# Performance work log

Measured on AMD Instinct MI355X. Metric: run time of the kernel, lower is better.

## Reference

```python
import jax, jax.numpy as jnp
from jax import lax
import numpy as np

IMG_CH = 3
C = 48            # total channels
HIDDEN = 256
FIRE_RATE = 0.5
DX_NOISE = 0.0
NEG_SLOPE = 0.01  # torch LeakyReLU default


def _dwconv(x_nchw, w):
    # depthwise 3x3 conv with reflect padding, w: [C,1,3,3]
    xp = jnp.pad(x_nchw, ((0, 0), (0, 0), (1, 1), (1, 1)), mode='reflect')
    return lax.conv_general_dilated(
        xp, w, window_strides=(1, 1), padding='VALID',
        feature_group_count=C,
        dimension_numbers=('NCHW', 'OIHW', 'NCHW'))


def setup_inputs() -> dict:
    key = jax.random.key(0)
    ks = jax.random.split(key, 6)
    x = jax.random.normal(ks[0], (8, 256, 256, C), dtype=jnp.float32)
    filt0 = jax.random.normal(ks[1], (C, 1, 3, 3), dtype=jnp.float32) * 0.1
    filt1 = jax.random.normal(ks[2], (C, 1, 3, 3), dtype=jnp.float32) * 0.1
    fan_in = 3 * C
    w1 = jax.random.normal(ks[3], (HIDDEN, 3 * C), dtype=jnp.float32) / np.sqrt(fan_in).astype(np.float32)
    b1 = jax.random.normal(ks[4], (HIDDEN,), dtype=jnp.float32) * 0.01
    # original zero-inits w2; randomized small so outputs/grads are nontrivial
    w2 = jax.random.normal(ks[5], (C, HIDDEN), dtype=jnp.float32) * 0.02
    return {"x": x, "filt0": filt0, "filt1": filt1, "w1": w1, "b1": b1, "w2": w2, "steps": 4}


def reference(x, filt0, filt1, w1, b1, w2, steps):
    ch_mask = (jnp.arange(C) >= IMG_CH).astype(x.dtype)  # immutable image channels
    rng = jax.random.key(42)
    for i in range(steps):
        xc = jnp.transpose(x, (0, 3, 1, 2))                       # [B,C,H,W]
        p = jnp.concatenate([xc, _dwconv(xc, filt0), _dwconv(xc, filt1)], axis=1)
        p = jnp.transpose(p, (0, 2, 3, 1))                        # [B,H,W,3C]
        h = jax.nn.leaky_relu(jnp.einsum('bhwf,of->bhwo', p, w1) + b1, NEG_SLOPE)
        d = jnp.einsum('bhwo,co->bhwc', h, w2)                    # [B,H,W,C]
        k1, k2 = jax.random.split(jax.random.fold_in(rng, i))
        fire = (jax.random.uniform(k1, d.shape[:3] + (1,)) > FIRE_RATE).astype(d.dtype)
        d = d * fire + DX_NOISE * jax.random.normal(k2, d.shape[:3] + (1,), dtype=d.dtype)
        d = d * ch_mask
        x = x + d
    return x
```

## Files before the change

### kernel.cpp

```cpp
#include <hip/hip_runtime.h>
#include <stdint.h>
#include <stddef.h>


#define B_   8
#define H_   256
#define W_   256
#define C_   48
#define F_   144
#define HID_ 256
#define PW_  64
#define NTOT (B_*H_*W_*C_)
#define XSTR 56

typedef __attribute__((ext_vector_type(8))) short short8;
typedef __attribute__((ext_vector_type(4))) float f32x4;

struct U2 { unsigned x, y; };

__host__ __device__ __forceinline__ unsigned rotl32(unsigned v, int r) {
  return (v << r) | (v >> (32 - r));
}

__host__ __device__ __forceinline__ U2 threefry2x32(unsigned k0, unsigned k1,
                                                    unsigned x0, unsigned x1) {
  const unsigned k2 = k0 ^ k1 ^ 0x1BD11BDAu;
  x0 += k0; x1 += k1;
#define TF_R(r) { x0 += x1; x1 = rotl32(x1, r); x1 ^= x0; }
  TF_R(13) TF_R(15) TF_R(26) TF_R(6)
  x0 += k1; x1 += k2 + 1u;
  TF_R(17) TF_R(29) TF_R(16) TF_R(24)
  x0 += k2; x1 += k0 + 2u;
  TF_R(13) TF_R(15) TF_R(26) TF_R(6)
  x0 += k0; x1 += k1 + 3u;
  TF_R(17) TF_R(29) TF_R(16) TF_R(24)
  x0 += k1; x1 += k2 + 4u;
  TF_R(13) TF_R(15) TF_R(26) TF_R(6)
  x0 += k2; x1 += k0 + 5u;
#undef TF_R
  U2 r; r.x = x0; r.y = x1; return r;
}

__device__ __forceinline__ unsigned short f2bf(float f) {
  unsigned u = __float_as_uint(f);
  unsigned r = u + 0x7FFFu + ((u >> 16) & 1u);
  return (unsigned short)(r >> 16);
}
__device__ __forceinline__ unsigned packbf2(float lo, float hi) {
  return (unsigned)f2bf(lo) | ((unsigned)f2bf(hi) << 16);
}
__device__ __forceinline__ float bf2f(unsigned short u) {
  return __uint_as_float(((unsigned)u) << 16);
}

#define W1B_N 114688
#define W2B_N 12288
__global__ void nca_pack(const float* __restrict__ w1,
                         const float* __restrict__ w2,
                         const float* __restrict__ f0,
                         const float* __restrict__ f1,
                         unsigned short* __restrict__ w1B,
                         unsigned short* __restrict__ w2B) {
  int i = blockIdx.x * 256 + threadIdx.x;
  if (i < W1B_N) {
    int ntg = i / 7168, r = i - ntg * 7168;
    int ks = r >> 9, r2 = r & 511;
    int lane = r2 >> 3, j = r2 & 7;
    int o = ntg * 16 + (lane & 15);
    int k = ks * 32 + (lane >> 4) * 8 + j;
    float v = 0.0f;
    if (k < 432) {
      int tap = k / 48, c = k - tap * 48;
      v = w1[o * F_ + 48 + c] * f0[c * 9 + tap]
        + w1[o * F_ + 96 + c] * f1[c * 9 + tap];
      if (tap == 4) v += w1[o * F_ + c];
    }
    w1B[i] = f2bf(v);
  }
  if (i < W2B_N) {
    int nt = i >> 12, r = i & 4095;
    int ks = r >> 9, r2 = r & 511;
    int lane = r2 >> 3, j = r2 & 7;
    int c = nt * 16 + (lane & 15);
    int o = ks * 32 + (lane >> 4) * 8 + j;
    w2B[i] = f2bf(w2[c * HID_ + o]);
  }
}

__device__ __forceinline__ int aoff(int chunk, int c16) {
  if (chunk > 53) chunk = 53;
  const int tap = chunk / 6;
  const int cst = (chunk - tap * 6) * 8;
  const int dy = tap / 3;
  const int dx = tap - dy * 3;
  return (dy * 66 + c16 + dx) * XSTR + cst;
}

template<int INBF, int OUTBF>
__global__ __launch_bounds__(256, 3)
void nca_step(const void* __restrict__ xin_, void* __restrict__ xout_,
              const unsigned short* __restrict__ w1B,
              const float* __restrict__ b1,
              const unsigned short* __restrict__ w2Bp,
              unsigned ka, unsigned kb) {
  __shared__ __align__(16) char smem[32768];
  __shared__ float fireL[PW_];
  short* xT = (short*)smem;
  short* hA = (short*)smem;

  const int t = threadIdx.x;
  const int bid = blockIdx.x;
  const int wseg = bid & 3;
  const int h = (bid >> 2) & 255;
  const int b = bid >> 10;
  const int w0 = wseg * PW_;
  const int gbase = ((b * H_ + h) * W_ + w0) * C_;

  if (t < PW_) {
    unsigned j = (unsigned)((b * H_ + h) * W_ + w0 + t);
    U2 r = threefry2x32(ka, kb, 0u, j);
    unsigned bits = r.x ^ r.y;
    fireL[t] = ((bits >> 9) > 4194304u) ? 1.0f : 0.0f;
  }
  {
    const int hr[3] = { (h == 0) ? 1 : h - 1, h, (h == 255) ? 254 : h + 1 };
#pragma unroll
    for (int g = 0; g < 10; ++g) {
      int i = t + g * 256;
      if (i < 2376) {
        int row = i / 792, rem = i - row * 792;
        int px = rem / 12, c4 = rem - px * 12;
        int w = w0 - 1 + px;
        int wg = (w < 0) ? 1 : (w > 255) ? 254 : w;
        const int gidx = ((b * H_ + hr[row]) * W_ + wg) * C_ + c4 * 4;
        uint2 d;
        if constexpr (INBF) {
          d = *(const uint2*)((const unsigned short*)xin_ + gidx);
        } else {
          const float4 v = *(const float4*)((const float*)xin_ + gidx);
          d.x = packbf2(v.x, v.y); d.y = packbf2(v.z, v.w);
        }
        *(uint2*)&xT[(row * 66 + px) * XSTR + c4 * 4] = d;
      }
    }
  }
  __syncthreads();

  const int wv = t >> 6, lane = t & 63;
  const int c16 = lane & 15, quad = lane >> 4;
  f32x4 acc[4][4];
#pragma unroll
  for (int mt = 0; mt < 4; ++mt)
#pragma unroll
    for (int nt = 0; nt < 4; ++nt) acc[mt][nt] = f32x4{0.f, 0.f, 0.f, 0.f};

#define LDA1(dst, ks) { const int o_ = aoff((ks) * 4 + quad, c16); \
  _Pragma("unroll") for (int mt = 0; mt < 4; ++mt) \
    dst[mt] = *(const short8*)&xT[o_ + mt * (16 * XSTR)]; }
#define LDB1(dst, ks) { _Pragma("unroll") for (int nt = 0; nt < 4; ++nt) \
  dst[nt] = *(const short8*)&w1B[((((wv * 4 + nt) * 14 + (ks)) << 6) | lane) << 3]; }
#define MM1(aa, bb) { _Pragma("unroll") for (int nt = 0; nt < 4; ++nt) \
  _Pragma("unroll") for (int mt = 0; mt < 4; ++mt) \
    acc[mt][nt] = __builtin_amdgcn_mfma_f32_16x16x32_bf16(aa[mt], bb[nt], acc[mt][nt], 0, 0, 0); }

  {
    short8 aA[4], aB[4], bA[4], bB[4];
    LDA1(aA, 0) LDB1(bA, 0)
#pragma unroll
    for (int kp = 0; kp < 7; ++kp) {
      LDA1(aB, 2 * kp + 1) LDB1(bB, 2 * kp + 1)
      MM1(aA, bA)
      if (kp < 6) { LDA1(aA, 2 * kp + 2) LDB1(bA, 2 * kp + 2) }
      MM1(aB, bB)
    }
  }
#undef LDA1
#undef LDB1
#undef MM1
  __syncthreads();

#pragma unroll
  for (int nt = 0; nt < 4; ++nt) {
    const int o = (wv * 4 + nt) * 16 + c16;
    const float bias = b1[o];
    const int ks2 = o >> 5, q2 = (o & 31) >> 3, j2 = o & 7;
#pragma unroll
    for (int mt = 0; mt < 4; ++mt) {
#pragma unroll
      for (int reg = 0; reg < 4; ++reg) {
        float z = acc[mt][nt][reg] + bias;
        z = (z >= 0.f) ? z : 0.01f * z;
        const int lane2 = (quad * 4 + reg) + (q2 << 4);
        hA[((((mt * 8 + ks2) << 6) | lane2) << 3) + j2] = (short)f2bf(z);
      }
    }
  }
  __syncthreads();

  {
    f32x4 acc2[3];
#pragma unroll
    for (int nt = 0; nt < 3; ++nt) acc2[nt] = f32x4{0.f, 0.f, 0.f, 0.f};

#define LDH2(dst, ks) dst = *(const short8*)&hA[(((wv * 8 + (ks)) << 6) | lane) << 3];
#define LDW2(dst, ks) { _Pragma("unroll") for (int nt = 0; nt < 3; ++nt) \
  dst[nt] = *(const short8*)&w2Bp[((((nt) * 8 + (ks)) << 6) | lane) << 3]; }
#define MM2(hh, ww) { _Pragma("unroll") for (int nt = 0; nt < 3; ++nt) \
  acc2[nt] = __builtin_amdgcn_mfma_f32_16x16x32_bf16(hh, ww[nt], acc2[nt], 0, 0, 0); }

    short8 hAx, hBx, cA[3], cB[3];
    LDH2(hAx, 0) LDW2(cA, 0)
#pragma unroll
    for (int kp = 0; kp < 4; ++kp) {
      LDH2(hBx, 2 * kp + 1) LDW2(cB, 2 * kp + 1)
      MM2(hAx, cA)
      if (kp < 3) { LDH2(hAx, 2 * kp + 2) LDW2(cA, 2 * kp + 2) }
      MM2(hBx, cB)
    }
#undef LDH2
#undef LDW2
#undef MM2

#pragma unroll
    for (int nt = 0; nt < 3; ++nt) {
      const int c = nt * 16 + c16;
#pragma unroll
      for (int reg = 0; reg < 4; ++reg) {
        const int pxl = wv * 16 + quad * 4 + reg;
        float d = acc2[nt][reg] * fireL[pxl];
        if (c < 3) d = 0.f;
        const int idx = gbase + pxl * C_ + c;
        float base;
        if constexpr (INBF) base = bf2f(((const unsigned short*)xin_)[idx]);
        else                base = ((const float*)xin_)[idx];
        const float r = base + d;
        if constexpr (OUTBF) ((unsigned short*)xout_)[idx] = f2bf(r);
        else                 ((float*)xout_)[idx] = r;
      }
    }
  }
}

extern "C" void kernel_launch(void* const* d_in, const int* in_sizes, int n_in,
                              void* d_out, int out_size, void* d_ws, size_t ws_size,
                              hipStream_t stream) {
  const float* xin = (const float*)d_in[0];
  const float* f0  = (const float*)d_in[1];
  const float* f1  = (const float*)d_in[2];
  const float* w1  = (const float*)d_in[3];
  const float* b1  = (const float*)d_in[4];
  const float* w2  = (const float*)d_in[5];
  float* xout = (float*)d_out;
  (void)in_sizes; (void)n_in; (void)out_size; (void)ws_size;

  unsigned ka[4], kb[4];
  for (int i = 0; i < 4; ++i) {
    U2 fold = threefry2x32(0u, 42u, 0u, (unsigned)i);
    U2 k1 = threefry2x32(fold.x, fold.y, 0u, 0u);
    ka[i] = k1.x; kb[i] = k1.y;
  }

  unsigned short* w1B = (unsigned short*)d_ws;
  unsigned short* w2B = w1B + W1B_N;
  unsigned short* xb  = (unsigned short*)((char*)d_ws + (size_t)(W1B_N + W2B_N) * 2);
  unsigned short* ob  = (unsigned short*)d_out;

  const dim3 gs(B_ * H_ * (W_ / PW_));
  const dim3 bs(256);

  nca_pack<<<(W1B_N + 255) / 256, 256, 0, stream>>>(w1, w2, f0, f1, w1B, w2B);
  nca_step<0, 1><<<gs, bs, 0, stream>>>(xin, xb,   w1B, b1, w2B, ka[0], kb[0]);
  nca_step<1, 1><<<gs, bs, 0, stream>>>(xb,  ob,   w1B, b1, w2B, ka[1], kb[1]);
  nca_step<1, 1><<<gs, bs, 0, stream>>>(ob,  xb,   w1B, b1, w2B, ka[2], kb[2]);
  nca_step<1, 0><<<gs, bs, 0, stream>>>(xb,  xout, w1B, b1, w2B, ka[3], kb[3]);
}
```

Before: 771.5 us.

## Deepen weight prefetch pipelines and reuse staged input tile for residual add

Unrolls both MFMA GEMM loops by hand and uses triple-buffered B-operand registers, so weight loads are issued two k-steps ahead of use. The first w2 fragments are now loaded before the barrier, overlapping the second GEMM's weight fetch with the activation stage. For bf16-input steps, the residual base value is read from the already staged shared-memory tile instead of global memory. The extra live registers could hurt occupancy under launch_bounds(256,3).

```diff
diff --git a/kernel.cpp b/kernel.cpp
--- a/kernel.cpp
+++ b/kernel.cpp
@@ -87,15 +87,6 @@
   }
 }
 
-__device__ __forceinline__ int aoff(int chunk, int c16) {
-  if (chunk > 53) chunk = 53;
-  const int tap = chunk / 6;
-  const int cst = (chunk - tap * 6) * 8;
-  const int dy = tap / 3;
-  const int dx = tap - dy * 3;
-  return (dy * 66 + c16 + dx) * XSTR + cst;
-}
-
 template<int INBF, int OUTBF>
 __global__ __launch_bounds__(256, 3)
 void nca_step(const void* __restrict__ xin_, void* __restrict__ xout_,
@@ -154,29 +145,59 @@
 #pragma unroll
     for (int nt = 0; nt < 4; ++nt) acc[mt][nt] = f32x4{0.f, 0.f, 0.f, 0.f};
 
-#define LDA1(dst, ks) { const int o_ = aoff((ks) * 4 + quad, c16); \
+#define LDA1(dst, ksl) { int ch_ = (ksl) * 4 + quad; \
+  if ((ksl) == 13 && ch_ > 53) ch_ = 53;  \
+  const int tap_ = ch_ / 6;    \
+  const int o_ = ((tap_ / 3) * 66 + c16 + (tap_ - (tap_ / 3) * 3)) * XSTR \
+                 + (ch_ - tap_ * 6) * 8; \
   _Pragma("unroll") for (int mt = 0; mt < 4; ++mt) \
     dst[mt] = *(const short8*)&xT[o_ + mt * (16 * XSTR)]; }
-#define LDB1(dst, ks) { _Pragma("unroll") for (int nt = 0; nt < 4; ++nt) \
-  dst[nt] = *(const short8*)&w1B[((((wv * 4 + nt) * 14 + (ks)) << 6) | lane) << 3]; }
+#define LDB1(dst, ksl) { _Pragma("unroll") for (int nt = 0; nt < 4; ++nt) \
+  dst[nt] = *(const short8*)&w1B[((((wv * 4 + nt) * 14 + (ksl)) << 6) | lane) << 3]; }
 #define MM1(aa, bb) { _Pragma("unroll") for (int nt = 0; nt < 4; ++nt) \
   _Pragma("unroll") for (int mt = 0; mt < 4; ++mt) \
     acc[mt][nt] = __builtin_amdgcn_mfma_f32_16x16x32_bf16(aa[mt], bb[nt], acc[mt][nt], 0, 0, 0); }
 
   {
-    short8 aA[4], aB[4], bA[4], bB[4];
-    LDA1(aA, 0) LDB1(bA, 0)
-#pragma unroll
-    for (int kp = 0; kp < 7; ++kp) {
-      LDA1(aB, 2 * kp + 1) LDB1(bB, 2 * kp + 1)
-      MM1(aA, bA)
-      if (kp < 6) { LDA1(aA, 2 * kp + 2) LDB1(bA, 2 * kp + 2) }
-      MM1(aB, bB)
-    }
+    short8 aP[4], aQ[4], bX[4], bY[4], bZ[4];
+    LDB1(bX, 0) LDB1(bY, 1) LDA1(aP, 0)
+    LDA1(aQ, 1)  LDB1(bZ, 2)   MM1(aP, bX)
+    LDA1(aP, 2)  LDB1(bX, 3)   MM1(aQ, bY)
+    LDA1(aQ, 3)  LDB1(bY, 4)   MM1(aP, bZ)
+    LDA1(aP, 4)  LDB1(bZ, 5)   MM1(aQ, bX)
+    LDA1(aQ, 5)  LDB1(bX, 6)   MM1(aP, bY)
+    LDA1(aP, 6)  LDB1(bY, 7)   MM1(aQ, bZ)
+    LDA1(aQ, 7)  LDB1(bZ, 8)   MM1(aP, bX)
+    LDA1(aP, 8)  LDB1(bX, 9)   MM1(aQ, bY)
+    LDA1(aQ, 9)  LDB1(bY, 10)  MM1(aP, bZ)
+    LDA1(aP, 10) LDB1(bZ, 11)  MM1(aQ, bX)
+    LDA1(aQ, 11) LDB1(bX, 12)  MM1(aP, bY)
+    LDA1(aP, 12) LDB1(bY, 13)  MM1(aQ, bZ)
+    LDA1(aQ, 13)               MM1(aP, bX)
+                               MM1(aQ, bY)
   }
 #undef LDA1
 #undef LDB1
 #undef MM1
+
+#define LDW2(dst, ksl) { _Pragma("unroll") for (int nt = 0; nt < 3; ++nt) \
+  dst[nt] = *(const short8*)&w2Bp[((((nt) * 8 + (ksl)) << 6) | lane) << 3]; }
+#define LDH2(dst, ksl) dst = *(const short8*)&hA[(((wv * 8 + (ksl)) << 6) | lane) << 3];
+#define MM2(hh, ww) { _Pragma("unroll") for (int nt = 0; nt < 3; ++nt) \
+  acc2[nt] = __builtin_amdgcn_mfma_f32_16x16x32_bf16(hh, ww[nt], acc2[nt], 0, 0, 0); }
+
+  short8 wA[3], wB[3], wC[3];
+  LDW2(wA, 0) LDW2(wB, 1)
+
+  unsigned short bs[3][4];
+  if constexpr (INBF) {
+#pragma unroll
+    for (int nt = 0; nt < 3; ++nt)
+#pragma unroll
+      for (int reg = 0; reg < 4; ++reg)
+        bs[nt][reg] = (unsigned short)
+          xT[(66 + 1 + wv * 16 + quad * 4 + reg) * XSTR + nt * 16 + c16];
+  }
   __syncthreads();
 
 #pragma unroll
@@ -202,24 +223,16 @@
 #pragma unroll
     for (int nt = 0; nt < 3; ++nt) acc2[nt] = f32x4{0.f, 0.f, 0.f, 0.f};
 
-#define LDH2(dst, ks) dst = *(const short8*)&hA[(((wv * 8 + (ks)) << 6) | lane) << 3];
-#define LDW2(dst, ks) { _Pragma("unroll") for (int nt = 0; nt < 3; ++nt) \
-  dst[nt] = *(const short8*)&w2Bp[((((nt) * 8 + (ks)) << 6) | lane) << 3]; }
-#define MM2(hh, ww) { _Pragma("unroll") for (int nt = 0; nt < 3; ++nt) \
-  acc2[nt] = __builtin_amdgcn_mfma_f32_16x16x32_bf16(hh, ww[nt], acc2[nt], 0, 0, 0); }
-
-    short8 hAx, hBx, cA[3], cB[3];
-    LDH2(hAx, 0) LDW2(cA, 0)
-#pragma unroll
-    for (int kp = 0; kp < 4; ++kp) {
-      LDH2(hBx, 2 * kp + 1) LDW2(cB, 2 * kp + 1)
-      MM2(hAx, cA)
-      if (kp < 3) { LDH2(hAx, 2 * kp + 2) LDW2(cA, 2 * kp + 2) }
-      MM2(hBx, cB)
-    }
-#undef LDH2
-#undef LDW2
-#undef MM2
+    short8 h0, h1;
+    LDH2(h0, 0)
+    LDH2(h1, 1) LDW2(wC, 2) MM2(h0, wA)
+    LDH2(h0, 2) LDW2(wA, 3) MM2(h1, wB)
+    LDH2(h1, 3) LDW2(wB, 4) MM2(h0, wC)
+    LDH2(h0, 4) LDW2(wC, 5) MM2(h1, wA)
+    LDH2(h1, 5) LDW2(wA, 6) MM2(h0, wB)
+    LDH2(h0, 6) LDW2(wB, 7) MM2(h1, wC)
+    LDH2(h1, 7)             MM2(h0, wA)
+                            MM2(h1, wB)
 
 #pragma unroll
     for (int nt = 0; nt < 3; ++nt) {
@@ -231,7 +244,7 @@
         if (c < 3) d = 0.f;
         const int idx = gbase + pxl * C_ + c;
         float base;
-        if constexpr (INBF) base = bf2f(((const unsigned short*)xin_)[idx]);
+        if constexpr (INBF) base = bf2f(bs[nt][reg]);
         else                base = ((const float*)xin_)[idx];
         const float r = base + d;
         if constexpr (OUTBF) ((unsigned short*)xout_)[idx] = f2bf(r);
@@ -239,6 +252,9 @@
       }
     }
   }
+#undef LDW2
+#undef LDH2
+#undef MM2
 }
 
 extern "C" void kernel_launch(void* const* d_in, const int* in_sizes, int n_in,
```

Result: slower. 821.6 us (+6.5%).
